# Performance work log

Hardware: AMD Instinct MI355X
Metric: run time of the kernel (lower is better)

## Reference

```python
import jax, jax.numpy as jnp
import numpy as np

V, I, H, OUT = 50000, 512, 1024, 2   # node_size, input_dim, hidden_dim, out_dim
P, L = 256, 64                       # num paths, max path length
NH = 32                              # num attention heads
HD = H // NH


def setup_inputs() -> dict:
    key = jax.random.key(0)
    ks = jax.random.split(key, 10)
    paths = jax.random.randint(ks[0], (P, L), 0, V)          # padded path token ids
    lengths = jax.random.randint(ks[1], (P,), 1, L + 1)       # true path lengths in [1, L]
    g = lambda k, shape, s: jax.random.normal(k, shape, jnp.float32) * s
    return {
        "paths": paths,
        "lengths": lengths,
        "emb_table": g(ks[2], (V, I), 0.1),
        "W_ih": g(ks[3], (4 * H, I), 0.02),
        "W_hh": g(ks[4], (4 * H, H), 0.02),
        "b_ih": jnp.zeros((4 * H,), jnp.float32),
        "b_hh": jnp.zeros((4 * H,), jnp.float32),
        "W_in": g(ks[5], (3 * H, H), 0.02),   # packed q,k,v in_proj (torch layout)
        "b_in": jnp.zeros((3 * H,), jnp.float32),
        "W_out": g(ks[6], (H, H), 0.02),
        "b_out": jnp.zeros((H,), jnp.float32),
        "W_lin": g(ks[7], (OUT, H), 0.02),
        "b_lin": jnp.zeros((OUT,), jnp.float32),
    }


def reference(paths, lengths, emb_table, W_ih, W_hh, b_ih, b_hh,
              W_in, b_in, W_out, b_out, W_lin, b_lin):
    p = paths.shape[0]
    x = emb_table[paths]                 # [P, L, I] (batched embedding of all ragged paths)
    xs = jnp.swapaxes(x, 0, 1)           # [L, P, I] time-major for scan
    b = b_ih + b_hh

    def step(carry, xt):                 # single-layer LSTM, torch gate order i,f,g,o
        h, c = carry
        gates = xt @ W_ih.T + h @ W_hh.T + b          # [P, 4H]
        i_g, f_g, g_g, o_g = jnp.split(gates, 4, axis=-1)
        c = jax.nn.sigmoid(f_g) * c + jax.nn.sigmoid(i_g) * jnp.tanh(g_g)
        h = jax.nn.sigmoid(o_g) * jnp.tanh(c)
        return (h, c), h

    h0 = jnp.zeros((p, H), x.dtype)
    _, hs = jax.lax.scan(step, (h0, h0), xs)          # [L, P, H]
    # final hidden of each path at its true length (equiv. to per-path h_n in the torch loop)
    final_h = hs[lengths - 1, jnp.arange(p)]          # [P, H]
    sum_hidden = final_h[None]                        # [1, P, H]  (seq=1, batch=P)

    # nn.MultiheadAttention(sum_hidden, sum_hidden, sum_hidden), seq_len = 1
    qkv = sum_hidden @ W_in.T + b_in                  # [1, P, 3H]
    q, k, v = jnp.split(qkv, 3, axis=-1)
    qh = q.reshape(1, p, NH, HD)
    kh = k.reshape(1, p, NH, HD)
    vh = v.reshape(1, p, NH, HD)
    scale = 1.0 / np.sqrt(HD).astype(np.float32)
    scores = jnp.einsum('qpnd,kpnd->pnqk', qh * scale, kh)   # [P, NH, 1, 1]
    attn = jax.nn.softmax(scores, axis=-1)
    ctx = jnp.einsum('pnqk,kpnd->qpnd', attn, vh).reshape(1, p, H)
    attn_out = ctx @ W_out.T + b_out                  # [1, P, H]

    # MaxPool2d((P,1)) on (C=1, H=P, W=hidden): max over the P paths
    pooled = jnp.max(attn_out, axis=1, keepdims=True)  # [1, 1, H]
    out = jax.nn.sigmoid(pooled @ W_lin.T + b_lin)     # [1, 1, OUT]
    return out
```

## Files before the change

### kernel.cpp

```cpp
#include <hip/hip_runtime.h>
#include <stdint.h>

typedef unsigned short u16;
typedef unsigned int u32;
typedef __attribute__((ext_vector_type(8))) short s16x8;
typedef __attribute__((ext_vector_type(4))) float f32x4;

#define P_ 256
#define L_ 64
#define IDIM 512
#define H_ 1024
#define PH (P_ * H_)

__device__ __forceinline__ u16 f2bf(float f){union{float f;u32 u;}v;v.f=f;u32 u=v.u;return (u16)((u+0x7FFFu+((u>>16)&1u))>>16);}
__device__ __forceinline__ float sigf(float x){return 1.0f/(1.0f+__expf(-x));}
__device__ __forceinline__ float tanhf_(float x){return 1.0f-2.0f/(__expf(2.0f*x)+1.0f);}

__device__ __forceinline__ s16x8 pack8v(float4 a, float4 b){
  s16x8 r;
  r[0]=(short)f2bf(a.x); r[1]=(short)f2bf(a.y); r[2]=(short)f2bf(a.z); r[3]=(short)f2bf(a.w);
  r[4]=(short)f2bf(b.x); r[5]=(short)f2bf(b.y); r[6]=(short)f2bf(b.z); r[7]=(short)f2bf(b.w);
  return r;
}
__device__ __forceinline__ s16x8 pack8(const float* s){
  return pack8v(*(const float4*)s, *(const float4*)(s+4));
}
__device__ __forceinline__ void st16_coh(u16* addr, s16x8 v){
  asm volatile("global_store_dwordx4 %0, %1, off sc0 sc1" :: "v"(addr), "v"(v) : "memory");
}
__device__ __forceinline__ void st_pair(u16* addr, float hv, int lane){
  u32 b = (u32)f2bf(hv);
  u32 other = __shfl_xor(b, 1);
  if ((lane & 1) == 0) {
    u32 w = b | (other << 16);
    __hip_atomic_store((u32*)addr, w, __ATOMIC_RELAXED, __HIP_MEMORY_SCOPE_AGENT);
  }
}
__device__ __forceinline__ void set_flag(u32* f, u32 v){
  __hip_atomic_store(f, v, __ATOMIC_RELAXED, __HIP_MEMORY_SCOPE_AGENT);
}
__device__ __forceinline__ void poll_flags(u32* fg, u32 target, int wid, int lane){
  if (wid == 0) {
    for (;;) {
      u32 f = __hip_atomic_load(&fg[lane], __ATOMIC_RELAXED, __HIP_MEMORY_SCOPE_AGENT);
      if (__all((int)(f >= target))) break;
      __builtin_amdgcn_s_sleep(1);
    }
  }
  asm volatile("" ::: "memory");
  __syncthreads();
}

__global__ void __launch_bounds__(256, 1)
tagger_net(const int* __restrict__ paths, const int* __restrict__ lengths,
           const float* __restrict__ emb,
           const float* __restrict__ Wih, const float* __restrict__ Whh,
           const float* __restrict__ bih, const float* __restrict__ bhh,
           const float* __restrict__ Win, const float* __restrict__ bin,
           const float* __restrict__ Wout, const float* __restrict__ bout,
           const float* __restrict__ Wlin, const float* __restrict__ blin,
           u16* __restrict__ X, u16* __restrict__ Hbuf,
           u16* __restrict__ vbuf, float* __restrict__ pmax,
           u32* flags, float* __restrict__ out)
{
  __shared__ __align__(16) float S[16384];
  const int tid  = threadIdx.x;
  const int wid  = tid >> 6, lane = tid & 63;
  const int lrow = lane & 15, lgrp = lane >> 4;
  const int bid  = blockIdx.x;
  const int g = bid & 3, jb = bid >> 2;
  const int p0 = g * 64, j0 = jb * 16;
  u32* fgrp = flags + g * 64;
  u32* myflag = fgrp + jb;

  for (int it = 0; it < 16; ++it) {
    int e = (it * 256 + tid) * 8;
    int row = e >> 9, col = e & 511;
    int tok = paths[(p0 + row) * L_ + jb];
    const float* s = emb + (size_t)tok * IDIM + col;
    float4 a = *(const float4*)s, b4 = *(const float4*)(s + 4);
    st16_coh(X + ((size_t)jb * P_ + p0 + row) * IDIM + col, pack8v(a, b4));
  }
#pragma unroll
  for (int i = 0; i < 2; ++i) {
    int idx = tid * 2 + i;
    int row = idx >> 3, cp = idx & 7;
    __hip_atomic_store((u32*)&Hbuf[(size_t)(p0 + row) * H_ + j0 + cp * 2], 0u,
                       __ATOMIC_RELAXED, __HIP_MEMORY_SCOPE_AGENT);
  }
  __syncthreads();
  if (tid == 0) set_flag(myflag, 1u);

  s16x8 breg[12][4];
#pragma unroll
  for (int i = 0; i < 12; ++i) {
    const int k = (wid + 4 * i) * 32 + lgrp * 8;
#pragma unroll
    for (int fn = 0; fn < 4; ++fn) {
      const int n = fn * H_ + j0 + lrow;
      const float* src = (k < IDIM) ? (Wih + (size_t)n * IDIM + k)
                                    : (Whh + (size_t)n * H_ + (k - IDIM));
      breg[i][fn] = pack8(src);
    }
  }

  const int prow = p0 + wid * 16 + lgrp * 4;
  int lenr[4]; float biasv[4];
#pragma unroll
  for (int r2 = 0; r2 < 4; ++r2) lenr[r2] = lengths[prow + r2];
#pragma unroll
  for (int fn = 0; fn < 4; ++fn) {
    int n = fn * H_ + j0 + lrow;
    biasv[fn] = bih[n] + bhh[n];
  }
  float cst[4] = {0.f,0.f,0.f,0.f}, hst[4] = {0.f,0.f,0.f,0.f};

  poll_flags(fgrp, 1u, wid, lane);

  const size_t aX = (size_t)(p0 + lrow) * IDIM + lgrp * 8;
  const size_t aH = (size_t)(p0 + lrow) * H_   + lgrp * 8;

  s16x8 fx[4][4];
#define LOADX(T) do { \
    const u16* Xt_ = X + (size_t)(T) * (P_ * IDIM) + aX; \
    _Pragma("unroll") \
    for (int i_ = 0; i_ < 4; ++i_) { \
      const int k0_ = wid * 32 + i_ * 128; \
      _Pragma("unroll") \
      for (int fm_ = 0; fm_ < 4; ++fm_) \
        fx[i_][fm_] = *(const s16x8*)(Xt_ + (size_t)fm_ * (16 * IDIM) + k0_); \
    } } while (0)

  LOADX(0);

  for (int t = 0; t < L_; ++t) {
    const u16* Hr = Hbuf + (size_t)t * PH;
    u16*       Hw = Hbuf + (size_t)(t + 1) * PH;

    f32x4 acc[4][4];
#pragma unroll
    for (int a = 0; a < 4; ++a)
#pragma unroll
      for (int b = 0; b < 4; ++b)
#pragma unroll
        for (int e = 0; e < 4; ++e) acc[a][b][e] = 0.0f;

#pragma unroll
    for (int i = 0; i < 4; ++i)
#pragma unroll
      for (int fm = 0; fm < 4; ++fm)
#pragma unroll
        for (int fn = 0; fn < 4; ++fn)
          acc[fm][fn] = __builtin_amdgcn_mfma_f32_16x16x32_bf16(fx[i][fm], breg[i][fn], acc[fm][fn], 0, 0, 0);

    poll_flags(fgrp, (u32)(t + 1), wid, lane);

    const u16* Hp = Hr + aH;
#pragma unroll
    for (int half = 0; half < 2; ++half) {
      s16x8 fh[4][4];
#pragma unroll
      for (int i = 0; i < 4; ++i) {
        const int kh = wid * 32 + (half * 4 + i) * 128;
#pragma unroll
        for (int fm = 0; fm < 4; ++fm)
          fh[i][fm] = *(const s16x8*)(Hp + (size_t)fm * (16 * H_) + kh);
      }
#pragma unroll
      for (int i = 0; i < 4; ++i)
#pragma unroll
        for (int fm = 0; fm < 4; ++fm)
#pragma unroll
          for (int fn = 0; fn < 4; ++fn)
            acc[fm][fn] = __builtin_amdgcn_mfma_f32_16x16x32_bf16(fh[i][fm], breg[4 + half * 4 + i][fn], acc[fm][fn], 0, 0, 0);
    }

    const int tp1 = (t < L_ - 1) ? (t + 1) : (L_ - 1);
    LOADX(tp1);

#pragma unroll
    for (int fm = 0; fm < 4; ++fm)
#pragma unroll
      for (int fn = 0; fn < 4; ++fn)
        *(f32x4*)&S[((wid * 16) + fm * 4 + fn) * 256 + lane * 4] = acc[fm][fn];
    __syncthreads();
    f32x4 red[4];
#pragma unroll
    for (int fn = 0; fn < 4; ++fn) {
      red[fn] = *(const f32x4*)&S[(wid * 4 + fn) * 256 + lane * 4];
#pragma unroll
      for (int w = 1; w < 4; ++w)
        red[fn] += *(const f32x4*)&S[(w * 16 + wid * 4 + fn) * 256 + lane * 4];
    }

#pragma unroll
    for (int r2 = 0; r2 < 4; ++r2) {
      if (t < lenr[r2]) {
        float gi = red[0][r2] + biasv[0];
        float gf = red[1][r2] + biasv[1];
        float gg = red[2][r2] + biasv[2];
        float go = red[3][r2] + biasv[3];
        float cn = sigf(gf) * cst[r2] + sigf(gi) * tanhf_(gg);
        cst[r2] = cn;
        hst[r2] = sigf(go) * tanhf_(cn);
      }
      st_pair(&Hw[(size_t)(prow + r2) * H_ + j0 + lrow], hst[r2], lane);
    }
    __syncthreads();
    if (tid == 0) set_flag(myflag, (u32)(t + 2));
  }

  const u16* hfin = Hbuf + (size_t)L_ * PH;
  poll_flags(fgrp, 65u, wid, lane);

  {
    f32x4 acc2[4];
#pragma unroll
    for (int a = 0; a < 4; ++a)
#pragma unroll
      for (int e = 0; e < 4; ++e) acc2[a][e] = 0.0f;
    const u16* hp = hfin + aH;
    const float* wv = Win + (size_t)(2 * H_ + j0 + lrow) * H_;
#pragma unroll
    for (int ic = 0; ic < 8; ++ic) {
      const int k0 = wid * 256 + ic * 32;
      s16x8 fbv = pack8(wv + k0 + lgrp * 8);
#pragma unroll
      for (int fm = 0; fm < 4; ++fm) {
        s16x8 fav = *(const s16x8*)(hp + (size_t)fm * (16 * H_) + k0);
        acc2[fm] = __builtin_amdgcn_mfma_f32_16x16x32_bf16(fav, fbv, acc2[fm], 0, 0, 0);
      }
    }
#pragma unroll
    for (int fm = 0; fm < 4; ++fm)
      *(f32x4*)&S[(wid * 4 + fm) * 256 + lane * 4] = acc2[fm];
    __syncthreads();
    f32x4 rv = *(const f32x4*)&S[(wid) * 256 + lane * 4];
#pragma unroll
    for (int w = 1; w < 4; ++w)
      rv += *(const f32x4*)&S[(w * 4 + wid) * 256 + lane * 4];
    float bvj = bin[2 * H_ + j0 + lrow];
#pragma unroll
    for (int r2 = 0; r2 < 4; ++r2)
      st_pair(&vbuf[(size_t)(prow + r2) * H_ + j0 + lrow], rv[r2] + bvj, lane);
  }
  __syncthreads();
  if (tid == 0) set_flag(myflag, 66u);
  poll_flags(fgrp, 66u, wid, lane);

  {
    f32x4 acc2[4];
#pragma unroll
    for (int a = 0; a < 4; ++a)
#pragma unroll
      for (int e = 0; e < 4; ++e) acc2[a][e] = 0.0f;
    const u16* vp = vbuf + aH;
    const float* wo = Wout + (size_t)(j0 + lrow) * H_;
#pragma unroll
    for (int ic = 0; ic < 8; ++ic) {
      const int k0 = wid * 256 + ic * 32;
      s16x8 fbv = pack8(wo + k0 + lgrp * 8);
#pragma unroll
      for (int fm = 0; fm < 4; ++fm) {
        s16x8 fav = *(const s16x8*)(vp + (size_t)fm * (16 * H_) + k0);
        acc2[fm] = __builtin_amdgcn_mfma_f32_16x16x32_bf16(fav, fbv, acc2[fm], 0, 0, 0);
      }
    }
#pragma unroll
    for (int fm = 0; fm < 4; ++fm)
      *(f32x4*)&S[(wid * 4 + fm) * 256 + lane * 4] = acc2[fm];
    __syncthreads();
    f32x4 rv = *(const f32x4*)&S[(wid) * 256 + lane * 4];
#pragma unroll
    for (int w = 1; w < 4; ++w)
      rv += *(const f32x4*)&S[(w * 4 + wid) * 256 + lane * 4];
    float bo = bout[j0 + lrow];
    float m = fmaxf(fmaxf(rv[0], rv[1]), fmaxf(rv[2], rv[3])) + bo;
    __syncthreads();
    S[(wid * 4 + lgrp) * 16 + lrow] = m;
    __syncthreads();
    if (tid < 16) {
      float mx = S[tid];
#pragma unroll
      for (int s2 = 1; s2 < 16; ++s2) mx = fmaxf(mx, S[s2 * 16 + tid]);
      __hip_atomic_store(&pmax[(size_t)g * H_ + j0 + tid], mx, __ATOMIC_RELAXED, __HIP_MEMORY_SCOPE_AGENT);
    }
  }
  __syncthreads();
  if (tid == 0) set_flag(myflag, 67u);

  if (bid != 0) return;

  if (wid == 0) {
    for (int g2 = 0; g2 < 4; ++g2) {
      for (;;) {
        u32 f = __hip_atomic_load(&flags[g2 * 64 + lane], __ATOMIC_RELAXED, __HIP_MEMORY_SCOPE_AGENT);
        if (__all((int)(f >= 67u))) break;
        __builtin_amdgcn_s_sleep(1);
      }
    }
  }
  asm volatile("" ::: "memory");
  __syncthreads();
  {
    int j4 = tid * 4;
    float s0 = 0.f, s1 = 0.f;
#pragma unroll
    for (int e = 0; e < 4; ++e) {
      float pv = pmax[j4 + e];
#pragma unroll
      for (int gg2 = 1; gg2 < 4; ++gg2) pv = fmaxf(pv, pmax[gg2 * H_ + j4 + e]);
      s0 += pv * Wlin[j4 + e];
      s1 += pv * Wlin[H_ + j4 + e];
    }
    S[tid] = s0; S[256 + tid] = s1;
    __syncthreads();
    for (int s2 = 128; s2 > 0; s2 >>= 1) {
      if (tid < s2) { S[tid] += S[tid + s2]; S[256 + tid] += S[256 + tid + s2]; }
      __syncthreads();
    }
    if (tid == 0) {
      out[0] = sigf(S[0] + blin[0]);
      out[1] = sigf(S[256] + blin[1]);
    }
  }
}

extern "C" void kernel_launch(void* const* d_in, const int* in_sizes, int n_in,
                              void* d_out, int out_size, void* d_ws, size_t ws_size,
                              hipStream_t stream) {
  const int*   paths   = (const int*)d_in[0];
  const int*   lengths = (const int*)d_in[1];
  const float* emb     = (const float*)d_in[2];
  const float* Wih     = (const float*)d_in[3];
  const float* Whh     = (const float*)d_in[4];
  const float* bih     = (const float*)d_in[5];
  const float* bhh     = (const float*)d_in[6];
  const float* Win     = (const float*)d_in[7];
  const float* bin     = (const float*)d_in[8];
  const float* Wout    = (const float*)d_in[9];
  const float* bout    = (const float*)d_in[10];
  const float* Wlin    = (const float*)d_in[11];
  const float* blin    = (const float*)d_in[12];
  float* out = (float*)d_out;

  char* ws = (char*)d_ws;
  u32*   flags  = (u32*)  (ws);
  float* pmax   = (float*)(ws + 4096);
  u16*   X      = (u16*)  (ws + 32768);
  u16*   Hbuf   = (u16*)  (ws + 16810240);
  u16*   vbuf   = (u16*)  (ws + 50888960);

  hipMemsetAsync(flags, 0, 1024, stream);
  tagger_net<<<256, 256, 0, stream>>>(paths, lengths, emb, Wih, Whh, bih, bhh,
                                      Win, bin, Wout, bout, Wlin, blin,
                                      X, Hbuf, vbuf, pmax, flags, out);
}
```

Baseline: 606.2 us.

## Interleave two path groups per block to overlap recurrence sync with compute

```diff
diff --git a/kernel.cpp b/kernel.cpp
--- a/kernel.cpp
+++ b/kernel.cpp
@@ -68,28 +68,35 @@
   const int wid  = tid >> 6, lane = tid & 63;
   const int lrow = lane & 15, lgrp = lane >> 4;
   const int bid  = blockIdx.x;
-  const int g = bid & 3, jb = bid >> 2;
-  const int p0 = g * 64, j0 = jb * 16;
-  u32* fgrp = flags + g * 64;
-  u32* myflag = fgrp + jb;
-
-  for (int it = 0; it < 16; ++it) {
-    int e = (it * 256 + tid) * 8;
-    int row = e >> 9, col = e & 511;
-    int tok = paths[(p0 + row) * L_ + jb];
-    const float* s = emb + (size_t)tok * IDIM + col;
-    float4 a = *(const float4*)s, b4 = *(const float4*)(s + 4);
-    st16_coh(X + ((size_t)jb * P_ + p0 + row) * IDIM + col, pack8v(a, b4));
-  }
-#pragma unroll
-  for (int i = 0; i < 2; ++i) {
-    int idx = tid * 2 + i;
-    int row = idx >> 3, cp = idx & 7;
-    __hip_atomic_store((u32*)&Hbuf[(size_t)(p0 + row) * H_ + j0 + cp * 2], 0u,
-                       __ATOMIC_RELAXED, __HIP_MEMORY_SCOPE_AGENT);
+  const int pairsel = bid & 1, jb = bid >> 1;
+  const int p0A = pairsel * 64, p0B = p0A + 128;
+  const int j0 = jb * 16;
+  u32* fgA = flags + pairsel * 64;
+  u32* fgB = flags + (pairsel + 2) * 64;
+  u32* mfA = fgA + jb;
+  u32* mfB = fgB + jb;
+
+#pragma unroll
+  for (int gh = 0; gh < 2; ++gh) {
+    const int pg = gh ? p0B : p0A;
+    for (int it = 0; it < 16; ++it) {
+      int e = (it * 256 + tid) * 8;
+      int row = e >> 9, col = e & 511;
+      int tok = paths[(pg + row) * L_ + jb];
+      const float* s = emb + (size_t)tok * IDIM + col;
+      st16_coh(X + ((size_t)jb * P_ + pg + row) * IDIM + col,
+               pack8v(*(const float4*)s, *(const float4*)(s + 4)));
+    }
+#pragma unroll
+    for (int i = 0; i < 2; ++i) {
+      int idx = tid * 2 + i;
+      int row = idx >> 3, cp = idx & 7;
+      __hip_atomic_store((u32*)&Hbuf[(size_t)(pg + row) * H_ + j0 + cp * 2], 0u,
+                         __ATOMIC_RELAXED, __HIP_MEMORY_SCOPE_AGENT);
+    }
   }
   __syncthreads();
-  if (tid == 0) set_flag(myflag, 1u);
+  if (tid == 0) { set_flag(mfA, 1u); set_flag(mfB, 1u); }
 
   s16x8 breg[12][4];
 #pragma unroll
@@ -104,190 +111,168 @@
     }
   }
 
-  const int prow = p0 + wid * 16 + lgrp * 4;
-  int lenr[4]; float biasv[4];
-#pragma unroll
-  for (int r2 = 0; r2 < 4; ++r2) lenr[r2] = lengths[prow + r2];
+  const int prow_off = wid * 16 + lgrp * 4;
+  int lenrA[4], lenrB[4]; float biasv[4];
+#pragma unroll
+  for (int r2 = 0; r2 < 4; ++r2) {
+    lenrA[r2] = lengths[p0A + prow_off + r2];
+    lenrB[r2] = lengths[p0B + prow_off + r2];
+  }
 #pragma unroll
   for (int fn = 0; fn < 4; ++fn) {
     int n = fn * H_ + j0 + lrow;
     biasv[fn] = bih[n] + bhh[n];
   }
-  float cst[4] = {0.f,0.f,0.f,0.f}, hst[4] = {0.f,0.f,0.f,0.f};
-
-  poll_flags(fgrp, 1u, wid, lane);
-
-  const size_t aX = (size_t)(p0 + lrow) * IDIM + lgrp * 8;
-  const size_t aH = (size_t)(p0 + lrow) * H_   + lgrp * 8;
-
-  s16x8 fx[4][4];
-#define LOADX(T) do { \
-    const u16* Xt_ = X + (size_t)(T) * (P_ * IDIM) + aX; \
-    _Pragma("unroll") \
-    for (int i_ = 0; i_ < 4; ++i_) { \
-      const int k0_ = wid * 32 + i_ * 128; \
-      _Pragma("unroll") \
-      for (int fm_ = 0; fm_ < 4; ++fm_) \
-        fx[i_][fm_] = *(const s16x8*)(Xt_ + (size_t)fm_ * (16 * IDIM) + k0_); \
-    } } while (0)
-
-  LOADX(0);
+  float cstA[4] = {0.f,0.f,0.f,0.f}, hstA[4] = {0.f,0.f,0.f,0.f};
+  float cstB[4] = {0.f,0.f,0.f,0.f}, hstB[4] = {0.f,0.f,0.f,0.f};
+
+#define PHASE(T, PG, FG, MF, CST, HST, LENR) do {                              \
+    poll_flags(FG, (u32)((T) + 1), wid, lane);                                 \
+    const u16* Xt_ = X + (size_t)(T) * (P_ * IDIM)                             \
+                     + (size_t)((PG) + lrow) * IDIM + lgrp * 8;                \
+    const u16* Hp_ = Hbuf + (size_t)(T) * PH                                   \
+                     + (size_t)((PG) + lrow) * H_ + lgrp * 8;                  \
+    u16* Hw_ = Hbuf + (size_t)((T) + 1) * PH;                                  \
+    f32x4 acc[4][4];                                                           \
+    _Pragma("unroll") for (int a_ = 0; a_ < 4; ++a_)                           \
+      _Pragma("unroll") for (int b_ = 0; b_ < 4; ++b_)                         \
+        _Pragma("unroll") for (int e_ = 0; e_ < 4; ++e_) acc[a_][b_][e_] = 0.f;\
+    s16x8 fx_[4][4];                                                           \
+    _Pragma("unroll") for (int i_ = 0; i_ < 4; ++i_) {                         \
+      const int k0_ = wid * 32 + i_ * 128;                                     \
+      _Pragma("unroll") for (int fm_ = 0; fm_ < 4; ++fm_)                      \
+        fx_[i_][fm_] = *(const s16x8*)(Xt_ + (size_t)fm_ * (16 * IDIM) + k0_); \
+    }                                                                          \
+    _Pragma("unroll") for (int i_ = 0; i_ < 4; ++i_)                           \
+      _Pragma("unroll") for (int fm_ = 0; fm_ < 4; ++fm_)                      \
+        _Pragma("unroll") for (int fn_ = 0; fn_ < 4; ++fn_)                    \
+          acc[fm_][fn_] = __builtin_amdgcn_mfma_f32_16x16x32_bf16(             \
+              fx_[i_][fm_], breg[i_][fn_], acc[fm_][fn_], 0, 0, 0);            \
+    _Pragma("unroll") for (int half_ = 0; half_ < 2; ++half_) {                \
+      s16x8 fh_[4][4];                                                         \
+      _Pragma("unroll") for (int i_ = 0; i_ < 4; ++i_) {                       \
+        const int kh_ = wid * 32 + (half_ * 4 + i_) * 128;                     \
+        _Pragma("unroll") for (int fm_ = 0; fm_ < 4; ++fm_)                    \
+          fh_[i_][fm_] = *(const s16x8*)(Hp_ + (size_t)fm_ * (16 * H_) + kh_); \
+      }                                                                        \
+      _Pragma("unroll") for (int i_ = 0; i_ < 4; ++i_)                         \
+        _Pragma("unroll") for (int fm_ = 0; fm_ < 4; ++fm_)                    \
+          _Pragma("unroll") for (int fn_ = 0; fn_ < 4; ++fn_)                  \
+            acc[fm_][fn_] = __builtin_amdgcn_mfma_f32_16x16x32_bf16(           \
+                fh_[i_][fm_], breg[4 + half_ * 4 + i_][fn_], acc[fm_][fn_],    \
+                0, 0, 0);                                                      \
+    }                                                                          \
+    _Pragma("unroll") for (int fm_ = 0; fm_ < 4; ++fm_)                        \
+      _Pragma("unroll") for (int fn_ = 0; fn_ < 4; ++fn_)                      \
+        *(f32x4*)&S[((wid * 16) + fm_ * 4 + fn_) * 256 + lane * 4]             \
+            = acc[fm_][fn_];                                                   \
+    __syncthreads();                                                           \
+    f32x4 red[4];                                                              \
+    _Pragma("unroll") for (int fn_ = 0; fn_ < 4; ++fn_) {                      \
+      red[fn_] = *(const f32x4*)&S[(wid * 4 + fn_) * 256 + lane * 4];          \
+      _Pragma("unroll") for (int w_ = 1; w_ < 4; ++w_)                         \
+        red[fn_] += *(const f32x4*)&S[(w_ * 16 + wid * 4 + fn_) * 256          \
+                                      + lane * 4];                             \
+    }                                                                          \
+    _Pragma("unroll") for (int r_ = 0; r_ < 4; ++r_) {                         \
+      if ((T) < (LENR)[r_]) {                                                  \
+        float gi = red[0][r_] + biasv[0];                                      \
+        float gf = red[1][r_] + biasv[1];                                      \
+        float gg = red[2][r_] + biasv[2];                                      \
+        float go = red[3][r_] + biasv[3];                                      \
+        float cn = sigf(gf) * (CST)[r_] + sigf(gi) * tanhf_(gg);               \
+        (CST)[r_] = cn;                                                        \
+        (HST)[r_] = sigf(go) * tanhf_(cn);                                     \
+      }                                                                        \
+      st_pair(&Hw_[(size_t)((PG) + prow_off + r_) * H_ + j0 + lrow],           \
+              (HST)[r_], lane);                                                \
+    }                                                                          \
+    __syncthreads();                                                           \
+    if (tid == 0) set_flag(MF, (u32)((T) + 2));                                \
+  } while (0)
 
   for (int t = 0; t < L_; ++t) {
-    const u16* Hr = Hbuf + (size_t)t * PH;
-    u16*       Hw = Hbuf + (size_t)(t + 1) * PH;
-
-    f32x4 acc[4][4];
-#pragma unroll
-    for (int a = 0; a < 4; ++a)
-#pragma unroll
-      for (int b = 0; b < 4; ++b)
-#pragma unroll
-        for (int e = 0; e < 4; ++e) acc[a][b][e] = 0.0f;
-
-#pragma unroll
-    for (int i = 0; i < 4; ++i)
-#pragma unroll
-      for (int fm = 0; fm < 4; ++fm)
-#pragma unroll
-        for (int fn = 0; fn < 4; ++fn)
-          acc[fm][fn] = __builtin_amdgcn_mfma_f32_16x16x32_bf16(fx[i][fm], breg[i][fn], acc[fm][fn], 0, 0, 0);
-
-    poll_flags(fgrp, (u32)(t + 1), wid, lane);
-
-    const u16* Hp = Hr + aH;
-#pragma unroll
-    for (int half = 0; half < 2; ++half) {
-      s16x8 fh[4][4];
-#pragma unroll
-      for (int i = 0; i < 4; ++i) {
-        const int kh = wid * 32 + (half * 4 + i) * 128;
-#pragma unroll
-        for (int fm = 0; fm < 4; ++fm)
-          fh[i][fm] = *(const s16x8*)(Hp + (size_t)fm * (16 * H_) + kh);
-      }
-#pragma unroll
-      for (int i = 0; i < 4; ++i)
-#pragma unroll
-        for (int fm = 0; fm < 4; ++fm)
-#pragma unroll
-          for (int fn = 0; fn < 4; ++fn)
-            acc[fm][fn] = __builtin_amdgcn_mfma_f32_16x16x32_bf16(fh[i][fm], breg[4 + half * 4 + i][fn], acc[fm][fn], 0, 0, 0);
-    }
-
-    const int tp1 = (t < L_ - 1) ? (t + 1) : (L_ - 1);
-    LOADX(tp1);
-
-#pragma unroll
-    for (int fm = 0; fm < 4; ++fm)
-#pragma unroll
-      for (int fn = 0; fn < 4; ++fn)
-        *(f32x4*)&S[((wid * 16) + fm * 4 + fn) * 256 + lane * 4] = acc[fm][fn];
-    __syncthreads();
-    f32x4 red[4];
-#pragma unroll
-    for (int fn = 0; fn < 4; ++fn) {
-      red[fn] = *(const f32x4*)&S[(wid * 4 + fn) * 256 + lane * 4];
-#pragma unroll
-      for (int w = 1; w < 4; ++w)
-        red[fn] += *(const f32x4*)&S[(w * 16 + wid * 4 + fn) * 256 + lane * 4];
-    }
-
-#pragma unroll
-    for (int r2 = 0; r2 < 4; ++r2) {
-      if (t < lenr[r2]) {
-        float gi = red[0][r2] + biasv[0];
-        float gf = red[1][r2] + biasv[1];
-        float gg = red[2][r2] + biasv[2];
-        float go = red[3][r2] + biasv[3];
-        float cn = sigf(gf) * cst[r2] + sigf(gi) * tanhf_(gg);
-        cst[r2] = cn;
-        hst[r2] = sigf(go) * tanhf_(cn);
-      }
-      st_pair(&Hw[(size_t)(prow + r2) * H_ + j0 + lrow], hst[r2], lane);
-    }
-    __syncthreads();
-    if (tid == 0) set_flag(myflag, (u32)(t + 2));
+    PHASE(t, p0A, fgA, mfA, cstA, hstA, lenrA);
+    PHASE(t, p0B, fgB, mfB, cstB, hstB, lenrB);
   }
 
   const u16* hfin = Hbuf + (size_t)L_ * PH;
-  poll_flags(fgrp, 65u, wid, lane);
-
-  {
-    f32x4 acc2[4];
-#pragma unroll
-    for (int a = 0; a < 4; ++a)
-#pragma unroll
-      for (int e = 0; e < 4; ++e) acc2[a][e] = 0.0f;
-    const u16* hp = hfin + aH;
-    const float* wv = Win + (size_t)(2 * H_ + j0 + lrow) * H_;
-#pragma unroll
-    for (int ic = 0; ic < 8; ++ic) {
-      const int k0 = wid * 256 + ic * 32;
-      s16x8 fbv = pack8(wv + k0 + lgrp * 8);
-#pragma unroll
-      for (int fm = 0; fm < 4; ++fm) {
-        s16x8 fav = *(const s16x8*)(hp + (size_t)fm * (16 * H_) + k0);
-        acc2[fm] = __builtin_amdgcn_mfma_f32_16x16x32_bf16(fav, fbv, acc2[fm], 0, 0, 0);
-      }
-    }
-#pragma unroll
-    for (int fm = 0; fm < 4; ++fm)
-      *(f32x4*)&S[(wid * 4 + fm) * 256 + lane * 4] = acc2[fm];
-    __syncthreads();
-    f32x4 rv = *(const f32x4*)&S[(wid) * 256 + lane * 4];
-#pragma unroll
-    for (int w = 1; w < 4; ++w)
-      rv += *(const f32x4*)&S[(w * 4 + wid) * 256 + lane * 4];
-    float bvj = bin[2 * H_ + j0 + lrow];
-#pragma unroll
-    for (int r2 = 0; r2 < 4; ++r2)
-      st_pair(&vbuf[(size_t)(prow + r2) * H_ + j0 + lrow], rv[r2] + bvj, lane);
-  }
-  __syncthreads();
-  if (tid == 0) set_flag(myflag, 66u);
-  poll_flags(fgrp, 66u, wid, lane);
-
-  {
-    f32x4 acc2[4];
-#pragma unroll
-    for (int a = 0; a < 4; ++a)
-#pragma unroll
-      for (int e = 0; e < 4; ++e) acc2[a][e] = 0.0f;
-    const u16* vp = vbuf + aH;
-    const float* wo = Wout + (size_t)(j0 + lrow) * H_;
-#pragma unroll
-    for (int ic = 0; ic < 8; ++ic) {
-      const int k0 = wid * 256 + ic * 32;
-      s16x8 fbv = pack8(wo + k0 + lgrp * 8);
-#pragma unroll
-      for (int fm = 0; fm < 4; ++fm) {
-        s16x8 fav = *(const s16x8*)(vp + (size_t)fm * (16 * H_) + k0);
-        acc2[fm] = __builtin_amdgcn_mfma_f32_16x16x32_bf16(fav, fbv, acc2[fm], 0, 0, 0);
-      }
-    }
-#pragma unroll
-    for (int fm = 0; fm < 4; ++fm)
-      *(f32x4*)&S[(wid * 4 + fm) * 256 + lane * 4] = acc2[fm];
-    __syncthreads();
-    f32x4 rv = *(const f32x4*)&S[(wid) * 256 + lane * 4];
-#pragma unroll
-    for (int w = 1; w < 4; ++w)
-      rv += *(const f32x4*)&S[(w * 4 + wid) * 256 + lane * 4];
-    float bo = bout[j0 + lrow];
-    float m = fmaxf(fmaxf(rv[0], rv[1]), fmaxf(rv[2], rv[3])) + bo;
-    __syncthreads();
-    S[(wid * 4 + lgrp) * 16 + lrow] = m;
-    __syncthreads();
-    if (tid < 16) {
-      float mx = S[tid];
-#pragma unroll
-      for (int s2 = 1; s2 < 16; ++s2) mx = fmaxf(mx, S[s2 * 16 + tid]);
-      __hip_atomic_store(&pmax[(size_t)g * H_ + j0 + tid], mx, __ATOMIC_RELAXED, __HIP_MEMORY_SCOPE_AGENT);
-    }
-  }
-  __syncthreads();
-  if (tid == 0) set_flag(myflag, 67u);
+  poll_flags(fgA, 65u, wid, lane);
+  poll_flags(fgB, 65u, wid, lane);
+
+#define VGEMM(PG) do {                                                         \
+    f32x4 a2[4];                                                               \
+    _Pragma("unroll") for (int a_ = 0; a_ < 4; ++a_)                           \
+      _Pragma("unroll") for (int e_ = 0; e_ < 4; ++e_) a2[a_][e_] = 0.f;       \
+    const u16* hp_ = hfin + (size_t)((PG) + lrow) * H_ + lgrp * 8;             \
+    const float* wv_ = Win + (size_t)(2 * H_ + j0 + lrow) * H_;                \
+    _Pragma("unroll") for (int ic_ = 0; ic_ < 8; ++ic_) {                      \
+      const int k0_ = wid * 256 + ic_ * 32;                                    \
+      s16x8 fb_ = pack8(wv_ + k0_ + lgrp * 8);                                 \
+      _Pragma("unroll") for (int fm_ = 0; fm_ < 4; ++fm_) {                    \
+        s16x8 fa_ = *(const s16x8*)(hp_ + (size_t)fm_ * (16 * H_) + k0_);      \
+        a2[fm_] = __builtin_amdgcn_mfma_f32_16x16x32_bf16(fa_, fb_, a2[fm_],   \
+                                                          0, 0, 0);            \
+      }                                                                        \
+    }                                                                          \
+    _Pragma("unroll") for (int fm_ = 0; fm_ < 4; ++fm_)                        \
+      *(f32x4*)&S[(wid * 4 + fm_) * 256 + lane * 4] = a2[fm_];                 \
+    __syncthreads();                                                           \
+    f32x4 rv_ = *(const f32x4*)&S[(wid) * 256 + lane * 4];                     \
+    _Pragma("unroll") for (int w_ = 1; w_ < 4; ++w_)                           \
+      rv_ += *(const f32x4*)&S[(w_ * 4 + wid) * 256 + lane * 4];               \
+    float bvj_ = bin[2 * H_ + j0 + lrow];                                      \
+    _Pragma("unroll") for (int r_ = 0; r_ < 4; ++r_)                           \
+      st_pair(&vbuf[(size_t)((PG) + prow_off + r_) * H_ + j0 + lrow],          \
+              rv_[r_] + bvj_, lane);                                           \
+    __syncthreads();                                                           \
+  } while (0)
+
+  VGEMM(p0A);
+  VGEMM(p0B);
+  if (tid == 0) { set_flag(mfA, 66u); set_flag(mfB, 66u); }
+  poll_flags(fgA, 66u, wid, lane);
+  poll_flags(fgB, 66u, wid, lane);
+
+#define ATTN(PG, GIDX) do {                                                    \
+    f32x4 a2[4];                                                               \
+    _Pragma("unroll") for (int a_ = 0; a_ < 4; ++a_)                           \
+      _Pragma("unroll") for (int e_ = 0; e_ < 4; ++e_) a2[a_][e_] = 0.f;       \
+    const u16* vp_ = vbuf + (size_t)((PG) + lrow) * H_ + lgrp * 8;             \
+    const float* wo_ = Wout + (size_t)(j0 + lrow) * H_;                        \
+    _Pragma("unroll") for (int ic_ = 0; ic_ < 8; ++ic_) {                      \
+      const int k0_ = wid * 256 + ic_ * 32;                                    \
+      s16x8 fb_ = pack8(wo_ + k0_ + lgrp * 8);                                 \
+      _Pragma("unroll") for (int fm_ = 0; fm_ < 4; ++fm_) {                    \
+        s16x8 fa_ = *(const s16x8*)(vp_ + (size_t)fm_ * (16 * H_) + k0_);      \
+        a2[fm_] = __builtin_amdgcn_mfma_f32_16x16x32_bf16(fa_, fb_, a2[fm_],   \
+                                                          0, 0, 0);            \
+      }                                                                        \
+    }                                                                          \
+    _Pragma("unroll") for (int fm_ = 0; fm_ < 4; ++fm_)                        \
+      *(f32x4*)&S[(wid * 4 + fm_) * 256 + lane * 4] = a2[fm_];                 \
+    __syncthreads();                                                           \
+    f32x4 rv_ = *(const f32x4*)&S[(wid) * 256 + lane * 4];                     \
+    _Pragma("unroll") for (int w_ = 1; w_ < 4; ++w_)                           \
+      rv_ += *(const f32x4*)&S[(w_ * 4 + wid) * 256 + lane * 4];               \
+    float m_ = fmaxf(fmaxf(rv_[0], rv_[1]), fmaxf(rv_[2], rv_[3]))             \
+               + bout[j0 + lrow];                                              \
+    __syncthreads();                                                           \
+    S[(wid * 4 + lgrp) * 16 + lrow] = m_;                                      \
+    __syncthreads();                                                           \
+    if (tid < 16) {                                                            \
+      float mx_ = S[tid];                                                      \
+      _Pragma("unroll") for (int s_ = 1; s_ < 16; ++s_)                        \
+        mx_ = fmaxf(mx_, S[s_ * 16 + tid]);                                    \
+      __hip_atomic_store(&pmax[(size_t)(GIDX) * H_ + j0 + tid], mx_,           \
+                         __ATOMIC_RELAXED, __HIP_MEMORY_SCOPE_AGENT);          \
+    }                                                                          \
+    __syncthreads();                                                           \
+  } while (0)
+
+  ATTN(p0A, pairsel);
+  ATTN(p0B, pairsel + 2);
+  if (tid == 0) { set_flag(mfA, 67u); set_flag(mfB, 67u); }
 
   if (bid != 0) return;
 
@@ -352,7 +337,7 @@
   u16*   vbuf   = (u16*)  (ws + 50888960);
 
   hipMemsetAsync(flags, 0, 1024, stream);
-  tagger_net<<<256, 256, 0, stream>>>(paths, lengths, emb, Wih, Whh, bih, bhh,
+  tagger_net<<<128, 256, 0, stream>>>(paths, lengths, emb, Wih, Whh, bih, bhh,
                                       Win, bin, Wout, bout, Wlin, blin,
                                       X, Hbuf, vbuf, pmax, flags, out);
 }
```

New measurement: 1.289 ms. 2.13x slower.

## Replace per-step flag barrier with sentinel-based data polling on hidden-state buffers

Applied to the files above, without the earlier changes.

```diff
diff --git a/kernel.cpp b/kernel.cpp
--- a/kernel.cpp
+++ b/kernel.cpp
@@ -5,6 +5,7 @@
 typedef unsigned int u32;
 typedef __attribute__((ext_vector_type(8))) short s16x8;
 typedef __attribute__((ext_vector_type(4))) float f32x4;
+typedef __attribute__((ext_vector_type(4))) unsigned int u32x4;
 
 #define P_ 256
 #define L_ 64
@@ -27,6 +28,15 @@
 }
 __device__ __forceinline__ void st16_coh(u16* addr, s16x8 v){
   asm volatile("global_store_dwordx4 %0, %1, off sc0 sc1" :: "v"(addr), "v"(v) : "memory");
+}
+__device__ __forceinline__ s16x8 ld16_coh(const u16* a){
+  s16x8 v;
+  asm volatile("global_load_dwordx4 %0, %1, off sc0 sc1" : "=v"(v) : "v"(a) : "memory");
+  return v;
+}
+__device__ __forceinline__ u32 frag_bad(s16x8 v){
+  u32x4 w = __builtin_bit_cast(u32x4, v);
+  return (u32)((w[0]==0xFFFFFFFFu)|(w[1]==0xFFFFFFFFu)|(w[2]==0xFFFFFFFFu)|(w[3]==0xFFFFFFFFu));
 }
 __device__ __forceinline__ void st_pair(u16* addr, float hv, int lane){
   u32 b = (u32)f2bf(hv);
@@ -78,8 +88,8 @@
     int row = e >> 9, col = e & 511;
     int tok = paths[(p0 + row) * L_ + jb];
     const float* s = emb + (size_t)tok * IDIM + col;
-    float4 a = *(const float4*)s, b4 = *(const float4*)(s + 4);
-    st16_coh(X + ((size_t)jb * P_ + p0 + row) * IDIM + col, pack8v(a, b4));
+    st16_coh(X + ((size_t)jb * P_ + p0 + row) * IDIM + col,
+             pack8v(*(const float4*)s, *(const float4*)(s + 4)));
   }
 #pragma unroll
   for (int i = 0; i < 2; ++i) {
@@ -87,6 +97,18 @@
     int row = idx >> 3, cp = idx & 7;
     __hip_atomic_store((u32*)&Hbuf[(size_t)(p0 + row) * H_ + j0 + cp * 2], 0u,
                        __ATOMIC_RELAXED, __HIP_MEMORY_SCOPE_AGENT);
+  }
+  {
+    s16x8 sv;
+#pragma unroll
+    for (int k2 = 0; k2 < 8; ++k2) sv[k2] = (short)0xFFFF;
+    for (int it = 0; it < 32; ++it) {
+      int idx = it * 256 + tid;
+      int buf = idx >> 7;
+      int rr  = (idx >> 1) & 63;
+      int cc  = (idx & 1) * 8;
+      st16_coh(Hbuf + (size_t)(buf + 1) * PH + (size_t)(p0 + rr) * H_ + j0 + cc, sv);
+    }
   }
   __syncthreads();
   if (tid == 0) set_flag(myflag, 1u);
@@ -153,18 +175,28 @@
         for (int fn = 0; fn < 4; ++fn)
           acc[fm][fn] = __builtin_amdgcn_mfma_f32_16x16x32_bf16(fx[i][fm], breg[i][fn], acc[fm][fn], 0, 0, 0);
 
-    poll_flags(fgrp, (u32)(t + 1), wid, lane);
-
     const u16* Hp = Hr + aH;
 #pragma unroll
     for (int half = 0; half < 2; ++half) {
       s16x8 fh[4][4];
-#pragma unroll
-      for (int i = 0; i < 4; ++i) {
-        const int kh = wid * 32 + (half * 4 + i) * 128;
-#pragma unroll
-        for (int fm = 0; fm < 4; ++fm)
-          fh[i][fm] = *(const s16x8*)(Hp + (size_t)fm * (16 * H_) + kh);
+      for (;;) {
+#pragma unroll
+        for (int i = 0; i < 4; ++i) {
+          const int kh = wid * 32 + (half * 4 + i) * 128;
+#pragma unroll
+          for (int fm = 0; fm < 4; ++fm)
+            fh[i][fm] = ld16_coh(Hp + (size_t)fm * (16 * H_) + kh);
+        }
+        asm volatile("s_waitcnt vmcnt(0)" ::: "memory");
+        __builtin_amdgcn_sched_barrier(0);
+        u32 bad = 0;
+#pragma unroll
+        for (int i = 0; i < 4; ++i)
+#pragma unroll
+          for (int fm = 0; fm < 4; ++fm)
+            bad |= frag_bad(fh[i][fm]);
+        if (!__any((int)bad)) break;
+        __builtin_amdgcn_s_sleep(2);
       }
 #pragma unroll
       for (int i = 0; i < 4; ++i)
@@ -207,11 +239,11 @@
       st_pair(&Hw[(size_t)(prow + r2) * H_ + j0 + lrow], hst[r2], lane);
     }
     __syncthreads();
-    if (tid == 0) set_flag(myflag, (u32)(t + 2));
-  }
-
+  }
+
+  if (tid == 0) set_flag(myflag, 2u);
   const u16* hfin = Hbuf + (size_t)L_ * PH;
-  poll_flags(fgrp, 65u, wid, lane);
+  poll_flags(fgrp, 2u, wid, lane);
 
   {
     f32x4 acc2[4];
@@ -245,8 +277,8 @@
       st_pair(&vbuf[(size_t)(prow + r2) * H_ + j0 + lrow], rv[r2] + bvj, lane);
   }
   __syncthreads();
-  if (tid == 0) set_flag(myflag, 66u);
-  poll_flags(fgrp, 66u, wid, lane);
+  if (tid == 0) set_flag(myflag, 3u);
+  poll_flags(fgrp, 3u, wid, lane);
 
   {
     f32x4 acc2[4];
@@ -287,7 +319,7 @@
     }
   }
   __syncthreads();
-  if (tid == 0) set_flag(myflag, 67u);
+  if (tid == 0) set_flag(myflag, 4u);
 
   if (bid != 0) return;
 
@@ -295,7 +327,7 @@
     for (int g2 = 0; g2 < 4; ++g2) {
       for (;;) {
         u32 f = __hip_atomic_load(&flags[g2 * 64 + lane], __ATOMIC_RELAXED, __HIP_MEMORY_SCOPE_AGENT);
-        if (__all((int)(f >= 67u))) break;
+        if (__all((int)(f >= 4u))) break;
         __builtin_amdgcn_s_sleep(1);
       }
     }
```

Result: no change. 616.0 us (+1.6%).

## Double block to 512 threads splitting LSTM K-reduction across eight waves

Applied to the files above, without the earlier changes.

```diff
diff --git a/kernel.cpp b/kernel.cpp
--- a/kernel.cpp
+++ b/kernel.cpp
@@ -50,8 +50,14 @@
   asm volatile("" ::: "memory");
   __syncthreads();
 }
-
-__global__ void __launch_bounds__(256, 1)
+__device__ __forceinline__ void lds_barrier(){
+  asm volatile("s_waitcnt lgkmcnt(0)" ::: "memory");
+  __builtin_amdgcn_sched_barrier(0);
+  __builtin_amdgcn_s_barrier();
+  __builtin_amdgcn_sched_barrier(0);
+}
+
+__global__ void __launch_bounds__(512, 1)
 tagger_net(const int* __restrict__ paths, const int* __restrict__ lengths,
            const float* __restrict__ emb,
            const float* __restrict__ Wih, const float* __restrict__ Whh,
@@ -73,38 +79,36 @@
   u32* fgrp = flags + g * 64;
   u32* myflag = fgrp + jb;
 
-  for (int it = 0; it < 16; ++it) {
-    int e = (it * 256 + tid) * 8;
+  for (int it = 0; it < 8; ++it) {
+    int e = (it * 512 + tid) * 8;
     int row = e >> 9, col = e & 511;
     int tok = paths[(p0 + row) * L_ + jb];
     const float* s = emb + (size_t)tok * IDIM + col;
-    float4 a = *(const float4*)s, b4 = *(const float4*)(s + 4);
-    st16_coh(X + ((size_t)jb * P_ + p0 + row) * IDIM + col, pack8v(a, b4));
-  }
-#pragma unroll
-  for (int i = 0; i < 2; ++i) {
-    int idx = tid * 2 + i;
-    int row = idx >> 3, cp = idx & 7;
+    st16_coh(X + ((size_t)jb * P_ + p0 + row) * IDIM + col,
+             pack8v(*(const float4*)s, *(const float4*)(s + 4)));
+  }
+  {
+    int row = tid >> 3, cp = tid & 7;
     __hip_atomic_store((u32*)&Hbuf[(size_t)(p0 + row) * H_ + j0 + cp * 2], 0u,
                        __ATOMIC_RELAXED, __HIP_MEMORY_SCOPE_AGENT);
   }
   __syncthreads();
   if (tid == 0) set_flag(myflag, 1u);
 
-  s16x8 breg[12][4];
-#pragma unroll
-  for (int i = 0; i < 12; ++i) {
-    const int k = (wid + 4 * i) * 32 + lgrp * 8;
+  s16x8 breg[6][4];
+#pragma unroll
+  for (int i = 0; i < 6; ++i) {
+    const int kg = (wid + 8 * i) * 32 + lgrp * 8;
 #pragma unroll
     for (int fn = 0; fn < 4; ++fn) {
       const int n = fn * H_ + j0 + lrow;
-      const float* src = (k < IDIM) ? (Wih + (size_t)n * IDIM + k)
-                                    : (Whh + (size_t)n * H_ + (k - IDIM));
+      const float* src = (kg < IDIM) ? (Wih + (size_t)n * IDIM + kg)
+                                     : (Whh + (size_t)n * H_ + (kg - IDIM));
       breg[i][fn] = pack8(src);
     }
   }
 
-  const int prow = p0 + wid * 16 + lgrp * 4;
+  const int prow = p0 + (wid & 3) * 16 + lgrp * 4;
   int lenr[4]; float biasv[4];
 #pragma unroll
   for (int r2 = 0; r2 < 4; ++r2) lenr[r2] = lengths[prow + r2];
@@ -120,12 +124,12 @@
   const size_t aX = (size_t)(p0 + lrow) * IDIM + lgrp * 8;
   const size_t aH = (size_t)(p0 + lrow) * H_   + lgrp * 8;
 
-  s16x8 fx[4][4];
+  s16x8 fx[2][4];
 #define LOADX(T) do { \
     const u16* Xt_ = X + (size_t)(T) * (P_ * IDIM) + aX; \
     _Pragma("unroll") \
-    for (int i_ = 0; i_ < 4; ++i_) { \
-      const int k0_ = wid * 32 + i_ * 128; \
+    for (int i_ = 0; i_ < 2; ++i_) { \
+      const int k0_ = (wid + 8 * i_) * 32; \
       _Pragma("unroll") \
       for (int fm_ = 0; fm_ < 4; ++fm_) \
         fx[i_][fm_] = *(const s16x8*)(Xt_ + (size_t)fm_ * (16 * IDIM) + k0_); \
@@ -146,7 +150,7 @@
         for (int e = 0; e < 4; ++e) acc[a][b][e] = 0.0f;
 
 #pragma unroll
-    for (int i = 0; i < 4; ++i)
+    for (int i = 0; i < 2; ++i)
 #pragma unroll
       for (int fm = 0; fm < 4; ++fm)
 #pragma unroll
@@ -156,55 +160,73 @@
     poll_flags(fgrp, (u32)(t + 1), wid, lane);
 
     const u16* Hp = Hr + aH;
-#pragma unroll
-    for (int half = 0; half < 2; ++half) {
-      s16x8 fh[4][4];
-#pragma unroll
-      for (int i = 0; i < 4; ++i) {
-        const int kh = wid * 32 + (half * 4 + i) * 128;
-#pragma unroll
-        for (int fm = 0; fm < 4; ++fm)
-          fh[i][fm] = *(const s16x8*)(Hp + (size_t)fm * (16 * H_) + kh);
-      }
-#pragma unroll
-      for (int i = 0; i < 4; ++i)
-#pragma unroll
-        for (int fm = 0; fm < 4; ++fm)
-#pragma unroll
-          for (int fn = 0; fn < 4; ++fn)
-            acc[fm][fn] = __builtin_amdgcn_mfma_f32_16x16x32_bf16(fh[i][fm], breg[4 + half * 4 + i][fn], acc[fm][fn], 0, 0, 0);
-    }
-
-    const int tp1 = (t < L_ - 1) ? (t + 1) : (L_ - 1);
-    LOADX(tp1);
-
-#pragma unroll
-    for (int fm = 0; fm < 4; ++fm)
-#pragma unroll
-      for (int fn = 0; fn < 4; ++fn)
-        *(f32x4*)&S[((wid * 16) + fm * 4 + fn) * 256 + lane * 4] = acc[fm][fn];
-    __syncthreads();
+    s16x8 fhA[2][4], fhB[2][4];
+#pragma unroll
+    for (int i = 0; i < 2; ++i) {
+      const int kh = wid * 32 + i * 256;
+#pragma unroll
+      for (int fm = 0; fm < 4; ++fm)
+        fhA[i][fm] = *(const s16x8*)(Hp + (size_t)fm * (16 * H_) + kh);
+    }
+#pragma unroll
+    for (int i = 0; i < 2; ++i) {
+      const int kh = wid * 32 + 512 + i * 256;
+#pragma unroll
+      for (int fm = 0; fm < 4; ++fm)
+        fhB[i][fm] = *(const s16x8*)(Hp + (size_t)fm * (16 * H_) + kh);
+    }
+#pragma unroll
+    for (int i = 0; i < 2; ++i)
+#pragma unroll
+      for (int fm = 0; fm < 4; ++fm)
+#pragma unroll
+        for (int fn = 0; fn < 4; ++fn)
+          acc[fm][fn] = __builtin_amdgcn_mfma_f32_16x16x32_bf16(fhA[i][fm], breg[2 + i][fn], acc[fm][fn], 0, 0, 0);
+    { const int tp1 = (t < L_ - 1) ? (t + 1) : (L_ - 1); LOADX(tp1); }
+#pragma unroll
+    for (int i = 0; i < 2; ++i)
+#pragma unroll
+      for (int fm = 0; fm < 4; ++fm)
+#pragma unroll
+        for (int fn = 0; fn < 4; ++fn)
+          acc[fm][fn] = __builtin_amdgcn_mfma_f32_16x16x32_bf16(fhB[i][fm], breg[4 + i][fn], acc[fm][fn], 0, 0, 0);
+
     f32x4 red[4];
 #pragma unroll
-    for (int fn = 0; fn < 4; ++fn) {
-      red[fn] = *(const f32x4*)&S[(wid * 4 + fn) * 256 + lane * 4];
-#pragma unroll
-      for (int w = 1; w < 4; ++w)
-        red[fn] += *(const f32x4*)&S[(w * 16 + wid * 4 + fn) * 256 + lane * 4];
-    }
-
-#pragma unroll
-    for (int r2 = 0; r2 < 4; ++r2) {
-      if (t < lenr[r2]) {
-        float gi = red[0][r2] + biasv[0];
-        float gf = red[1][r2] + biasv[1];
-        float gg = red[2][r2] + biasv[2];
-        float go = red[3][r2] + biasv[3];
-        float cn = sigf(gf) * cst[r2] + sigf(gi) * tanhf_(gg);
-        cst[r2] = cn;
-        hst[r2] = sigf(go) * tanhf_(cn);
-      }
-      st_pair(&Hw[(size_t)(prow + r2) * H_ + j0 + lrow], hst[r2], lane);
+    for (int rr = 0; rr < 2; ++rr) {
+#pragma unroll
+      for (int fm = 0; fm < 4; ++fm)
+#pragma unroll
+        for (int q = 0; q < 2; ++q)
+          *(f32x4*)&S[(wid * 8 + fm * 2 + q) * 256 + lane * 4] = acc[fm][2 * rr + q];
+      lds_barrier();
+      if (wid < 4) {
+#pragma unroll
+        for (int q = 0; q < 2; ++q) {
+          f32x4 v = *(const f32x4*)&S[(wid * 2 + q) * 256 + lane * 4];
+#pragma unroll
+          for (int s = 1; s < 8; ++s)
+            v += *(const f32x4*)&S[(s * 8 + wid * 2 + q) * 256 + lane * 4];
+          red[2 * rr + q] = v;
+        }
+      }
+      lds_barrier();
+    }
+
+    if (wid < 4) {
+#pragma unroll
+      for (int r2 = 0; r2 < 4; ++r2) {
+        if (t < lenr[r2]) {
+          float gi = red[0][r2] + biasv[0];
+          float gf = red[1][r2] + biasv[1];
+          float gg = red[2][r2] + biasv[2];
+          float go = red[3][r2] + biasv[3];
+          float cn = sigf(gf) * cst[r2] + sigf(gi) * tanhf_(gg);
+          cst[r2] = cn;
+          hst[r2] = sigf(go) * tanhf_(cn);
+        }
+        st_pair(&Hw[(size_t)(prow + r2) * H_ + j0 + lrow], hst[r2], lane);
+      }
     }
     __syncthreads();
     if (tid == 0) set_flag(myflag, (u32)(t + 2));
@@ -222,8 +244,8 @@
     const u16* hp = hfin + aH;
     const float* wv = Win + (size_t)(2 * H_ + j0 + lrow) * H_;
 #pragma unroll
-    for (int ic = 0; ic < 8; ++ic) {
-      const int k0 = wid * 256 + ic * 32;
+    for (int ic = 0; ic < 4; ++ic) {
+      const int k0 = wid * 128 + ic * 32;
       s16x8 fbv = pack8(wv + k0 + lgrp * 8);
 #pragma unroll
       for (int fm = 0; fm < 4; ++fm) {
@@ -235,14 +257,16 @@
     for (int fm = 0; fm < 4; ++fm)
       *(f32x4*)&S[(wid * 4 + fm) * 256 + lane * 4] = acc2[fm];
     __syncthreads();
-    f32x4 rv = *(const f32x4*)&S[(wid) * 256 + lane * 4];
-#pragma unroll
-    for (int w = 1; w < 4; ++w)
-      rv += *(const f32x4*)&S[(w * 4 + wid) * 256 + lane * 4];
-    float bvj = bin[2 * H_ + j0 + lrow];
-#pragma unroll
-    for (int r2 = 0; r2 < 4; ++r2)
-      st_pair(&vbuf[(size_t)(prow + r2) * H_ + j0 + lrow], rv[r2] + bvj, lane);
+    if (wid < 4) {
+      f32x4 rv = *(const f32x4*)&S[(wid) * 256 + lane * 4];
+#pragma unroll
+      for (int s = 1; s < 8; ++s)
+        rv += *(const f32x4*)&S[(s * 4 + wid) * 256 + lane * 4];
+      float bvj = bin[2 * H_ + j0 + lrow];
+#pragma unroll
+      for (int r2 = 0; r2 < 4; ++r2)
+        st_pair(&vbuf[(size_t)(prow + r2) * H_ + j0 + lrow], rv[r2] + bvj, lane);
+    }
   }
   __syncthreads();
   if (tid == 0) set_flag(myflag, 66u);
@@ -257,8 +281,8 @@
     const u16* vp = vbuf + aH;
     const float* wo = Wout + (size_t)(j0 + lrow) * H_;
 #pragma unroll
-    for (int ic = 0; ic < 8; ++ic) {
-      const int k0 = wid * 256 + ic * 32;
+    for (int ic = 0; ic < 4; ++ic) {
+      const int k0 = wid * 128 + ic * 32;
       s16x8 fbv = pack8(wo + k0 + lgrp * 8);
 #pragma unroll
       for (int fm = 0; fm < 4; ++fm) {
@@ -270,14 +294,18 @@
     for (int fm = 0; fm < 4; ++fm)
       *(f32x4*)&S[(wid * 4 + fm) * 256 + lane * 4] = acc2[fm];
     __syncthreads();
-    f32x4 rv = *(const f32x4*)&S[(wid) * 256 + lane * 4];
-#pragma unroll
-    for (int w = 1; w < 4; ++w)
-      rv += *(const f32x4*)&S[(w * 4 + wid) * 256 + lane * 4];
-    float bo = bout[j0 + lrow];
-    float m = fmaxf(fmaxf(rv[0], rv[1]), fmaxf(rv[2], rv[3])) + bo;
-    __syncthreads();
-    S[(wid * 4 + lgrp) * 16 + lrow] = m;
+    if (wid < 4) {
+      f32x4 rv = *(const f32x4*)&S[(wid) * 256 + lane * 4];
+#pragma unroll
+      for (int s = 1; s < 8; ++s)
+        rv += *(const f32x4*)&S[(s * 4 + wid) * 256 + lane * 4];
+      float bo = bout[j0 + lrow];
+      float m = fmaxf(fmaxf(rv[0], rv[1]), fmaxf(rv[2], rv[3])) + bo;
+      __syncthreads();
+      S[(wid * 4 + lgrp) * 16 + lrow] = m;
+    } else {
+      __syncthreads();
+    }
     __syncthreads();
     if (tid < 16) {
       float mx = S[tid];
@@ -303,25 +331,25 @@
   asm volatile("" ::: "memory");
   __syncthreads();
   {
-    int j4 = tid * 4;
+    int j2 = tid * 2;
     float s0 = 0.f, s1 = 0.f;
 #pragma unroll
-    for (int e = 0; e < 4; ++e) {
-      float pv = pmax[j4 + e];
-#pragma unroll
-      for (int gg2 = 1; gg2 < 4; ++gg2) pv = fmaxf(pv, pmax[gg2 * H_ + j4 + e]);
-      s0 += pv * Wlin[j4 + e];
-      s1 += pv * Wlin[H_ + j4 + e];
-    }
-    S[tid] = s0; S[256 + tid] = s1;
-    __syncthreads();
-    for (int s2 = 128; s2 > 0; s2 >>= 1) {
-      if (tid < s2) { S[tid] += S[tid + s2]; S[256 + tid] += S[256 + tid + s2]; }
+    for (int e = 0; e < 2; ++e) {
+      float pv = pmax[j2 + e];
+#pragma unroll
+      for (int gg2 = 1; gg2 < 4; ++gg2) pv = fmaxf(pv, pmax[gg2 * H_ + j2 + e]);
+      s0 += pv * Wlin[j2 + e];
+      s1 += pv * Wlin[H_ + j2 + e];
+    }
+    S[tid] = s0; S[512 + tid] = s1;
+    __syncthreads();
+    for (int s2 = 256; s2 > 0; s2 >>= 1) {
+      if (tid < s2) { S[tid] += S[tid + s2]; S[512 + tid] += S[512 + tid + s2]; }
       __syncthreads();
     }
     if (tid == 0) {
       out[0] = sigf(S[0] + blin[0]);
-      out[1] = sigf(S[256] + blin[1]);
+      out[1] = sigf(S[512] + blin[1]);
     }
   }
 }
@@ -352,7 +380,7 @@
   u16*   vbuf   = (u16*)  (ws + 50888960);
 
   hipMemsetAsync(flags, 0, 1024, stream);
-  tagger_net<<<256, 256, 0, stream>>>(paths, lengths, emb, Wih, Whh, bih, bhh,
+  tagger_net<<<256, 512, 0, stream>>>(paths, lengths, emb, Wih, Whh, bih, bhh,
                                       Win, bin, Wout, bout, Wlin, blin,
                                       X, Hbuf, vbuf, pmax, flags, out);
 }
```

New measurement: 553.9 us. 8.6% less time.
